# Kernel optimization log

Hardware: AMD Instinct MI355X
Metric: run time of the kernel (lower is better)

## Reference

```python
import jax, jax.numpy as jnp
import numpy as np

B, N, X_DIM, Y_DIM = 256, 128, 8, 8
Z_DIM, R_DIM, HID = 64, 128, 256
STEPS = 50
SIGMA_SQ = 0.5 ** 2
EPSILON = 1.0


def setup_inputs() -> dict:
    key = jax.random.key(0)
    ks = jax.random.split(key, 20)
    s = lambda fan_in: 1.0 / np.sqrt(fan_in)
    inp = {
        'x_ctx': jax.random.normal(ks[0], (B, N, X_DIM), jnp.float32),
        'y_ctx': jax.random.normal(ks[1], (B, N, Y_DIM), jnp.float32),
        'mask': jnp.ones((B, N, 1), jnp.float32),
        'z0': jax.random.normal(ks[2], (B, Z_DIM), jnp.float32),
        'noise': jax.random.normal(ks[3], (STEPS, B, Z_DIM), jnp.float32),
        # encoder: pointwise MLP on [x,y] then masked mean pool, project to r_dim
        'We1': jax.random.normal(ks[4], (X_DIM + Y_DIM, HID), jnp.float32) * s(X_DIM + Y_DIM),
        'be1': jnp.zeros((HID,), jnp.float32),
        'We2': jax.random.normal(ks[5], (HID, R_DIM), jnp.float32) * s(HID),
        'be2': jnp.zeros((R_DIM,), jnp.float32),
        # decoder: MLP([x, z]) -> y per context point
        'Wd1': jax.random.normal(ks[6], (X_DIM + Z_DIM, HID), jnp.float32) * s(X_DIM + Z_DIM),
        'bd1': jnp.zeros((HID,), jnp.float32),
        'Wd2': jax.random.normal(ks[7], (HID, Y_DIM), jnp.float32) * s(HID),
        'bd2': jnp.zeros((Y_DIM,), jnp.float32),
        # drift net: MLP([z, r, t]) -> z_dim
        'Wb1': jax.random.normal(ks[8], (Z_DIM + R_DIM + 1, HID), jnp.float32) * s(Z_DIM + R_DIM + 1),
        'bb1': jnp.zeros((HID,), jnp.float32),
        'Wb2': jax.random.normal(ks[9], (HID, Z_DIM), jnp.float32) * s(HID),
        'bb2': jnp.zeros((Z_DIM,), jnp.float32),
    }
    return inp


def _encode(x, y, mask, We1, be1, We2, be2):
    phi = jax.nn.gelu(jnp.concatenate([x, y], axis=-1) @ We1 + be1)  # [B,N,H]
    pooled = (phi * mask).sum(axis=1) / jnp.maximum(mask.sum(axis=1), 1.0)  # [B,H]
    return pooled @ We2 + be2  # [B,R]


def _decode(z, x, Wd1, bd1, Wd2, bd2):
    zb = jnp.broadcast_to(z[:, None, :], (z.shape[0], x.shape[1], z.shape[1]))
    h = jax.nn.gelu(jnp.concatenate([x, zb], axis=-1) @ Wd1 + bd1)  # [B,N,H]
    return h @ Wd2 + bd2  # [B,N,Y]


def _drift(z, r, t_col, Wb1, bb1, Wb2, bb2):
    h = jax.nn.gelu(jnp.concatenate([z, r, t_col], axis=-1) @ Wb1 + bb1)
    return h @ Wb2 + bb2  # [B,Z]


def reference(x_ctx, y_ctx, mask, z0, noise,
              We1, be1, We2, be2, Wd1, bd1, Wd2, bd2, Wb1, bb1, Wb2, bb2):
    dt = 1.0 / STEPS
    r = _encode(x_ctx, y_ctx, mask, We1, be1, We2, be2)  # [B,R]

    def energy_sum(z, t):
        u0 = 0.5 * jnp.sum(z ** 2, axis=1)  # [B]
        mu_y = _decode(z, x_ctx, Wd1, bd1, Wd2, bd2)
        sse = jnp.sum(((y_ctx - mu_y) ** 2) * mask, axis=(1, 2))  # [B]
        u1 = 0.5 * sse / SIGMA_SQ + u0
        return jnp.sum((1.0 - t) * u0 + t * u1)

    grad_energy = jax.grad(energy_sum, argnums=0)
    t_steps = (jnp.arange(STEPS, dtype=jnp.float32) * dt)
    noise_scale = jnp.sqrt(jnp.float32(2.0 * EPSILON * dt))

    def step(z, xs):
        t_curr, eps_noise = xs
        grad_u = jnp.clip(grad_energy(z, t_curr), -100.0, 100.0)
        t_col = jnp.full((z.shape[0], 1), t_curr, dtype=z.dtype)
        b = _drift(z, r, t_col, Wb1, bb1, Wb2, bb2)
        dz = (-EPSILON * grad_u + b) * dt + noise_scale * eps_noise
        return z + dz, None

    z_final, _ = jax.lax.scan(step, z0, (t_steps, noise))
    return z_final
```

## Files before the change

kernel.cpp:

```cpp
#include <hip/hip_runtime.h>
#include <math.h>

#define BB    256
#define NN_   128
#define ZD    64
#define RD    128
#define HID   256
#define NSTEPS 50
#define NT    16
#define NTILES 8
#define TPB   512
#define PADD  258

__device__ __forceinline__ double fast_exp_d(double x) {
    const double L2E   = 1.44269504088896340736;
    const double LN2HI = 6.93147180369123816490e-01;
    const double LN2LO = 1.90821492927058770002e-10;
    const double MAGIC = 6755399441055744.0;
    double vn = fma(x, L2E, MAGIC);
    int ni = __double2loint(vn);
    double n = vn - MAGIC;
    double r = fma(n, -LN2HI, x);
    r = fma(n, -LN2LO, r);
    double p = 2.50521083854417187751e-08;
    p = fma(p, r, 2.75573192239858906526e-07);
    p = fma(p, r, 2.75573192239858906526e-06);
    p = fma(p, r, 2.48015873015873015873e-05);
    p = fma(p, r, 1.98412698412698412698e-04);
    p = fma(p, r, 1.38888888888888888889e-03);
    p = fma(p, r, 8.33333333333333333333e-03);
    p = fma(p, r, 4.16666666666666666667e-02);
    p = fma(p, r, 1.66666666666666666667e-01);
    p = fma(p, r, 0.5);
    p = fma(p, r, 1.0);
    p = fma(p, r, 1.0);
    return p * __hiloint2double((1023 + ni) << 20, 0);
}

__device__ __forceinline__ double sigmoid_d(double w) {
    double wc = fmin(fmax(w, -60.0), 60.0);
    double e = fast_exp_d(-wc);
    double d = 1.0 + e;
    float r0 = __builtin_amdgcn_rcpf((float)d);
    double y = (double)r0;
    y = fma(y, fma(-d, y, 1.0), y);
    y = fma(y, fma(-d, y, 1.0), y);
    return y;
}

__device__ __forceinline__ double gelu_d(double x) {
    const double c2 = 1.59576912160573071176;
    double w = c2 * x * fma(0.044715, x * x, 1.0);
    return x * sigmoid_d(w);
}

__device__ __forceinline__ void gelu_both_d(double x, double& h, double& gp) {
    const double c  = 0.79788456080286535588;
    const double a  = 0.044715;
    double x2 = x * x;
    double w  = (2.0 * c) * x * fma(a, x2, 1.0);
    double hp = sigmoid_d(w);
    h = x * hp;
    double s = hp * (1.0 - hp);
    gp = fma(x * s, (2.0 * c) * fma(3.0 * a, x2, 1.0), hp);
}

struct Smem {
    double h_t[NT][PADD];
    float  wd2t_f[8][PADD];
    double z_ds[ZD];
    double hb_ds[HID];
    double scratch2[2][HID];
    double pmgz[512];
    double res_r[NT][8];
    double bp_d[8][ZD];
    double bd2_d[8];
    double bb2_d[ZD];
    double hbt_s[HID];
    double wbt_s[HID];
    float  bd1_s[HID];
    float  gp_t[NT][HID];
    float  x_s[NN_][8];
    float  y_s[NN_][8];
    float  m_s[NN_];
    __align__(16) float4 wd1z4[HID][16];
};

__global__ void __launch_bounds__(TPB)
nets_sampler_kernel(
    const float* __restrict__ x_ctx, const float* __restrict__ y_ctx,
    const float* __restrict__ mask,  const float* __restrict__ z0,
    const float* __restrict__ noise,
    const float* __restrict__ We1, const float* __restrict__ be1,
    const float* __restrict__ We2, const float* __restrict__ be2,
    const float* __restrict__ Wd1, const float* __restrict__ bd1,
    const float* __restrict__ Wd2, const float* __restrict__ bd2,
    const float* __restrict__ Wb1, const float* __restrict__ bb1,
    const float* __restrict__ Wb2, const float* __restrict__ bb2,
    float* __restrict__ out)
{
    extern __shared__ char smem_raw[];
    Smem& sm = *reinterpret_cast<Smem*>(smem_raw);

    const int b   = blockIdx.x;
    const int tid = threadIdx.x;
    const int j   = tid & 255;
    const int g   = tid >> 8;
    double* r_d = &sm.res_r[0][0];

    if (tid < 256) {
        reinterpret_cast<float4*>(&sm.x_s[0][0])[tid] =
            reinterpret_cast<const float4*>(x_ctx + (size_t)b * NN_ * 8)[tid];
        reinterpret_cast<float4*>(&sm.y_s[0][0])[tid] =
            reinterpret_cast<const float4*>(y_ctx + (size_t)b * NN_ * 8)[tid];
        sm.bd1_s[j] = bd1[j];
    }
    if (tid < NN_) sm.m_s[tid] = mask[(size_t)b * NN_ + tid];
    if (tid < ZD) {
        sm.z_ds[tid]  = (double)z0[(size_t)b * ZD + tid];
        sm.bb2_d[tid] = (double)bb2[tid];
    }
    if (tid < 8) sm.bd2_d[tid] = (double)bd2[tid];

#pragma unroll
    for (int kk = 0; kk < 32; kk++) {
        const int k = g * 32 + kk;
        const float v = Wd1[(8 + k) * HID + j];
        reinterpret_cast<float*>(&sm.wd1z4[j][0])[4 * ((k >> 2) ^ (j & 15)) + (k & 3)] = v;
    }

    float wd1x[8];
#pragma unroll
    for (int k = 0; k < 8; k++) wd1x[k] = Wd1[k * HID + j];

    const int du_k = tid & 63, du_c = tid >> 6;

    if (g == 0) {
        float4 a0 = reinterpret_cast<const float4*>(Wd2 + (size_t)j * 8)[0];
        float4 a1 = reinterpret_cast<const float4*>(Wd2 + (size_t)j * 8)[1];
        sm.wd2t_f[0][j] = a0.x; sm.wd2t_f[1][j] = a0.y;
        sm.wd2t_f[2][j] = a0.z; sm.wd2t_f[3][j] = a0.w;
        sm.wd2t_f[4][j] = a1.x; sm.wd2t_f[5][j] = a1.y;
        sm.wd2t_f[6][j] = a1.z; sm.wd2t_f[7][j] = a1.w;
    }

    __syncthreads();

    if (tid < 256) {
        float we1r[16];
#pragma unroll
        for (int k = 0; k < 16; k++) we1r[k] = We1[k * HID + j];
        double be1_d = (double)be1[j];
        double msum = 0.0;
        for (int n = 0; n < NN_; n++) msum += (double)sm.m_s[n];
        msum = fmax(msum, 1.0);
        double pacc = 0.0;
        for (int n = 0; n < NN_; n++) {
            double pre = be1_d;
#pragma unroll
            for (int k = 0; k < 8; k++) pre = fma((double)sm.x_s[n][k], (double)we1r[k], pre);
#pragma unroll
            for (int k = 0; k < 8; k++) pre = fma((double)sm.y_s[n][k], (double)we1r[8 + k], pre);
            pacc += gelu_d(pre) * (double)sm.m_s[n];
        }
        sm.hb_ds[j] = pacc / msum;
    }
    __syncthreads();
    if (tid < 256) {
        int i = tid & 127, half = tid >> 7;
        double racc = 0.0;
        for (int jj = half * 128; jj < half * 128 + 128; jj++)
            racc = fma(sm.hb_ds[jj], (double)We2[jj * RD + i], racc);
        sm.scratch2[half][i] = racc;
    }
    __syncthreads();
    if (tid < RD) r_d[tid] = sm.scratch2[0][tid] + sm.scratch2[1][tid] + (double)be2[tid];
    __syncthreads();

    if (tid < 256) {
        double hbr = (double)bb1[j];
        for (int k = 0; k < RD; k++)
            hbr = fma(r_d[k], (double)Wb1[(ZD + k) * HID + j], hbr);
        sm.hbt_s[j] = hbr;
        sm.wbt_s[j] = (double)Wb1[(ZD + RD) * HID + j];
    }
    __syncthreads();

    const double dt  = 1.0 / (double)NSTEPS;
    const double nsc = sqrt(2.0 * 1.0 * dt);

    for (int s = 0; s < NSTEPS; s++) {
        const double t = (double)s * dt;

        float nzf = 0.0f;
        if (tid < ZD) nzf = noise[((size_t)s * BB + b) * ZD + tid];

        double zd0 = 0.0, zd1 = 0.0;
#pragma unroll 4
        for (int q = 0; q < 16; q++) {
            float4 wv = sm.wd1z4[j][q ^ (j & 15)];
            const int k = q * 4;
            zd0 = fma(sm.z_ds[k],     (double)wv.x, zd0);
            zd1 = fma(sm.z_ds[k + 1], (double)wv.y, zd1);
            zd0 = fma(sm.z_ds[k + 2], (double)wv.z, zd0);
            zd1 = fma(sm.z_ds[k + 3], (double)wv.w, zd1);
        }
        const double zpre = (double)sm.bd1_s[j] + zd0 + zd1;

        {
            double a0 = 0.0;
            const int kb = g * 32;
            const float* wb1p = Wb1 + kb * HID + j;
#pragma unroll 8
            for (int kk = 0; kk < 32; kk++)
                a0 = fma(sm.z_ds[kb + kk], (double)wb1p[kk * HID], a0);
            sm.scratch2[g][j] = a0;
        }
        __syncthreads();
        if (tid < 256) {
            double hacc = sm.hbt_s[j] + t * sm.wbt_s[j]
                        + sm.scratch2[0][j] + sm.scratch2[1][j];
            sm.hb_ds[j] = gelu_d(hacc);
        }
        __syncthreads();
        {
            double acc = 0.0;
            const float* wb2p = Wb2 + (du_c * 32) * ZD + du_k;
#pragma unroll 8
            for (int i = 0; i < 32; i++)
                acc = fma(sm.hb_ds[du_c * 32 + i], (double)wb2p[i * ZD], acc);
            sm.bp_d[du_c][du_k] = acc;
        }

        double S = 0.0;
        for (int tile = 0; tile < NTILES; tile++) {
            const int base = tile * NT;
            const int rb = g * 8;
#pragma unroll 2
            for (int nn = 0; nn < 8; nn++) {
                const int row = rb + nn;
                const float4 xa = *reinterpret_cast<const float4*>(&sm.x_s[base + row][0]);
                const float4 xb = *reinterpret_cast<const float4*>(&sm.x_s[base + row][4]);
                double pre = zpre;
                pre = fma((double)xa.x, (double)wd1x[0], pre);
                pre = fma((double)xa.y, (double)wd1x[1], pre);
                pre = fma((double)xa.z, (double)wd1x[2], pre);
                pre = fma((double)xa.w, (double)wd1x[3], pre);
                pre = fma((double)xb.x, (double)wd1x[4], pre);
                pre = fma((double)xb.y, (double)wd1x[5], pre);
                pre = fma((double)xb.z, (double)wd1x[6], pre);
                pre = fma((double)xb.w, (double)wd1x[7], pre);
                double h, gp;
                gelu_both_d(pre, h, gp);
                sm.h_t[row][j]  = h;
                sm.gp_t[row][j] = (float)gp;
            }
            __syncthreads();
            {
                const int q = tid >> 7, pair = tid & 127;
                const int nn = pair >> 3, yd = pair & 7;
                const double2* hrow = reinterpret_cast<const double2*>(&sm.h_t[nn][q * 64]);
                const float2*  wrow = reinterpret_cast<const float2*>(&sm.wd2t_f[yd][q * 64]);
                double a0 = 0.0, a1 = 0.0;
#pragma unroll 8
                for (int i = 0; i < 32; i++) {
                    double2 hv = hrow[i];
                    float2  wv = wrow[i];
                    a0 = fma(hv.x, (double)wv.x, a0);
                    a1 = fma(hv.y, (double)wv.y, a1);
                }
                sm.pmgz[q * 128 + pair] = a0 + a1;
            }
            __syncthreads();
            if (tid < 128) {
                const int nn = tid >> 3, yd = tid & 7;
                double mu = sm.pmgz[tid] + sm.pmgz[128 + tid] + sm.pmgz[256 + tid]
                          + sm.pmgz[384 + tid] + sm.bd2_d[yd];
                sm.res_r[nn][yd] = 4.0 * t * (mu - (double)sm.y_s[base + nn][yd])
                                           * (double)sm.m_s[base + nn];
            }
            __syncthreads();
            {
                const float w0 = sm.wd2t_f[0][j], w1 = sm.wd2t_f[1][j];
                const float w2 = sm.wd2t_f[2][j], w3 = sm.wd2t_f[3][j];
                const float w4 = sm.wd2t_f[4][j], w5 = sm.wd2t_f[5][j];
                const float w6 = sm.wd2t_f[6][j], w7 = sm.wd2t_f[7][j];
                const int rb2 = g * 8;
#pragma unroll 2
                for (int nn = 0; nn < 8; nn++) {
                    const int row = rb2 + nn;
                    const double2* rr = reinterpret_cast<const double2*>(&sm.res_r[row][0]);
                    double2 r0 = rr[0], r1 = rr[1], r2 = rr[2], r3 = rr[3];
                    double dh = r0.x * (double)w0 + r0.y * (double)w1
                              + r1.x * (double)w2 + r1.y * (double)w3
                              + r2.x * (double)w4 + r2.y * (double)w5
                              + r3.x * (double)w6 + r3.y * (double)w7;
                    S = fma(dh, (double)sm.gp_t[row][j], S);
                }
            }
            __syncthreads();
        }

        sm.scratch2[g][j] = S;
        __syncthreads();
        {
            const int k = du_k, c = du_c;
            const int qk = k >> 2, ck = k & 3;
            double acc = 0.0;
#pragma unroll 8
            for (int i = 0; i < 32; i++) {
                const int jj = c * 32 + i;
                const float w = reinterpret_cast<const float*>(&sm.wd1z4[jj][0])
                                    [4 * (qk ^ (jj & 15)) + ck];
                const double sv = sm.scratch2[0][jj] + sm.scratch2[1][jj];
                acc = fma(sv, (double)w, acc);
            }
            sm.pmgz[c * 64 + k] = acc;
        }
        __syncthreads();
        if (tid < ZD) {
            double gsum = sm.z_ds[tid];
#pragma unroll
            for (int c = 0; c < 8; c++) gsum += sm.pmgz[c * 64 + tid];
            gsum = fmin(fmax(gsum, -100.0), 100.0);
            double bdr = sm.bb2_d[tid];
#pragma unroll
            for (int c = 0; c < 8; c++) bdr += sm.bp_d[c][tid];
            sm.z_ds[tid] = sm.z_ds[tid] + (bdr - gsum) * dt + nsc * (double)nzf;
        }
        __syncthreads();
    }

    if (tid < ZD) out[(size_t)b * ZD + tid] = (float)sm.z_ds[tid];
}

extern "C" void kernel_launch(void* const* d_in, const int* in_sizes, int n_in,
                              void* d_out, int out_size, void* d_ws, size_t ws_size,
                              hipStream_t stream) {
    const float* x_ctx = (const float*)d_in[0];
    const float* y_ctx = (const float*)d_in[1];
    const float* maskp = (const float*)d_in[2];
    const float* z0    = (const float*)d_in[3];
    const float* noise = (const float*)d_in[4];
    const float* We1   = (const float*)d_in[5];
    const float* be1   = (const float*)d_in[6];
    const float* We2   = (const float*)d_in[7];
    const float* be2   = (const float*)d_in[8];
    const float* Wd1   = (const float*)d_in[9];
    const float* bd1   = (const float*)d_in[10];
    const float* Wd2   = (const float*)d_in[11];
    const float* bd2   = (const float*)d_in[12];
    const float* Wb1   = (const float*)d_in[13];
    const float* bb1   = (const float*)d_in[14];
    const float* Wb2   = (const float*)d_in[15];
    const float* bb2   = (const float*)d_in[16];
    float* out = (float*)d_out;

    (void)hipFuncSetAttribute((const void*)nets_sampler_kernel,
                              hipFuncAttributeMaxDynamicSharedMemorySize,
                              (int)sizeof(Smem));

    nets_sampler_kernel<<<BB, TPB, sizeof(Smem), stream>>>(
        x_ctx, y_ctx, maskp, z0, noise,
        We1, be1, We2, be2, Wd1, bd1, Wd2, bd2, Wb1, bb1, Wb2, bb2, out);
}
```

Baseline: 1.859 ms.

## Double block size to 1024 threads and repartition per-step work

```diff
diff --git a/kernel.cpp b/kernel.cpp
--- a/kernel.cpp
+++ b/kernel.cpp
@@ -9,7 +9,7 @@
 #define NSTEPS 50
 #define NT    16
 #define NTILES 8
-#define TPB   512
+#define TPB   1024
 #define PADD  258
 
 __device__ __forceinline__ double fast_exp_d(double x) {
@@ -70,16 +70,15 @@
     float  wd2t_f[8][PADD];
     double z_ds[ZD];
     double hb_ds[HID];
-    double scratch2[2][HID];
-    double pmgz[512];
+    double scratch4[4][HID];
+    double pmgz[1024];
     double res_r[NT][8];
-    double bp_d[8][ZD];
+    double bp_d[16][ZD];
     double bd2_d[8];
     double bb2_d[ZD];
     double hbt_s[HID];
     double wbt_s[HID];
     float  bd1_s[HID];
-    float  gp_t[NT][HID];
     float  x_s[NN_][8];
     float  y_s[NN_][8];
     float  m_s[NN_];
@@ -105,7 +104,8 @@
     const int b   = blockIdx.x;
     const int tid = threadIdx.x;
     const int j   = tid & 255;
-    const int g   = tid >> 8;
+    const int q2  = tid >> 8;
+    const int du_k = tid & 63, du_c = tid >> 6;
     double* r_d = &sm.res_r[0][0];
 
     if (tid < 256) {
@@ -114,28 +114,6 @@
         reinterpret_cast<float4*>(&sm.y_s[0][0])[tid] =
             reinterpret_cast<const float4*>(y_ctx + (size_t)b * NN_ * 8)[tid];
         sm.bd1_s[j] = bd1[j];
-    }
-    if (tid < NN_) sm.m_s[tid] = mask[(size_t)b * NN_ + tid];
-    if (tid < ZD) {
-        sm.z_ds[tid]  = (double)z0[(size_t)b * ZD + tid];
-        sm.bb2_d[tid] = (double)bb2[tid];
-    }
-    if (tid < 8) sm.bd2_d[tid] = (double)bd2[tid];
-
-#pragma unroll
-    for (int kk = 0; kk < 32; kk++) {
-        const int k = g * 32 + kk;
-        const float v = Wd1[(8 + k) * HID + j];
-        reinterpret_cast<float*>(&sm.wd1z4[j][0])[4 * ((k >> 2) ^ (j & 15)) + (k & 3)] = v;
-    }
-
-    float wd1x[8];
-#pragma unroll
-    for (int k = 0; k < 8; k++) wd1x[k] = Wd1[k * HID + j];
-
-    const int du_k = tid & 63, du_c = tid >> 6;
-
-    if (g == 0) {
         float4 a0 = reinterpret_cast<const float4*>(Wd2 + (size_t)j * 8)[0];
         float4 a1 = reinterpret_cast<const float4*>(Wd2 + (size_t)j * 8)[1];
         sm.wd2t_f[0][j] = a0.x; sm.wd2t_f[1][j] = a0.y;
@@ -143,6 +121,23 @@
         sm.wd2t_f[4][j] = a1.x; sm.wd2t_f[5][j] = a1.y;
         sm.wd2t_f[6][j] = a1.z; sm.wd2t_f[7][j] = a1.w;
     }
+    if (tid < NN_) sm.m_s[tid] = mask[(size_t)b * NN_ + tid];
+    if (tid < ZD) {
+        sm.z_ds[tid]  = (double)z0[(size_t)b * ZD + tid];
+        sm.bb2_d[tid] = (double)bb2[tid];
+    }
+    if (tid < 8) sm.bd2_d[tid] = (double)bd2[tid];
+
+#pragma unroll
+    for (int kk = 0; kk < 16; kk++) {
+        const int k = q2 * 16 + kk;
+        const float v = Wd1[(8 + k) * HID + j];
+        reinterpret_cast<float*>(&sm.wd1z4[j][0])[4 * ((k >> 2) ^ (j & 15)) + (k & 3)] = v;
+    }
+
+    float wd1x[8];
+#pragma unroll
+    for (int k = 0; k < 8; k++) wd1x[k] = Wd1[k * HID + j];
 
     __syncthreads();
 
@@ -171,10 +166,10 @@
         double racc = 0.0;
         for (int jj = half * 128; jj < half * 128 + 128; jj++)
             racc = fma(sm.hb_ds[jj], (double)We2[jj * RD + i], racc);
-        sm.scratch2[half][i] = racc;
+        sm.scratch4[half][i] = racc;
     }
     __syncthreads();
-    if (tid < RD) r_d[tid] = sm.scratch2[0][tid] + sm.scratch2[1][tid] + (double)be2[tid];
+    if (tid < RD) r_d[tid] = sm.scratch4[0][tid] + sm.scratch4[1][tid] + (double)be2[tid];
     __syncthreads();
 
     if (tid < 256) {
@@ -209,61 +204,101 @@
 
         {
             double a0 = 0.0;
-            const int kb = g * 32;
+            const int kb = q2 * 16;
             const float* wb1p = Wb1 + kb * HID + j;
 #pragma unroll 8
-            for (int kk = 0; kk < 32; kk++)
+            for (int kk = 0; kk < 16; kk++)
                 a0 = fma(sm.z_ds[kb + kk], (double)wb1p[kk * HID], a0);
-            sm.scratch2[g][j] = a0;
+            sm.scratch4[q2][j] = a0;
         }
         __syncthreads();
         if (tid < 256) {
             double hacc = sm.hbt_s[j] + t * sm.wbt_s[j]
-                        + sm.scratch2[0][j] + sm.scratch2[1][j];
+                        + sm.scratch4[0][j] + sm.scratch4[1][j]
+                        + sm.scratch4[2][j] + sm.scratch4[3][j];
             sm.hb_ds[j] = gelu_d(hacc);
         }
         __syncthreads();
         {
             double acc = 0.0;
-            const float* wb2p = Wb2 + (du_c * 32) * ZD + du_k;
+            const float* wb2p = Wb2 + (du_c * 16) * ZD + du_k;
 #pragma unroll 8
-            for (int i = 0; i < 32; i++)
-                acc = fma(sm.hb_ds[du_c * 32 + i], (double)wb2p[i * ZD], acc);
+            for (int i = 0; i < 16; i++)
+                acc = fma(sm.hb_ds[du_c * 16 + i], (double)wb2p[i * ZD], acc);
             sm.bp_d[du_c][du_k] = acc;
         }
 
         double S = 0.0;
+        const int rb = q2 * 4;
+        float gp_r0, gp_r1, gp_r2, gp_r3;
+
         for (int tile = 0; tile < NTILES; tile++) {
-            const int base = tile * NT;
-            const int rb = g * 8;
-#pragma unroll 2
-            for (int nn = 0; nn < 8; nn++) {
-                const int row = rb + nn;
-                const float4 xa = *reinterpret_cast<const float4*>(&sm.x_s[base + row][0]);
-                const float4 xb = *reinterpret_cast<const float4*>(&sm.x_s[base + row][4]);
-                double pre = zpre;
-                pre = fma((double)xa.x, (double)wd1x[0], pre);
-                pre = fma((double)xa.y, (double)wd1x[1], pre);
-                pre = fma((double)xa.z, (double)wd1x[2], pre);
-                pre = fma((double)xa.w, (double)wd1x[3], pre);
-                pre = fma((double)xb.x, (double)wd1x[4], pre);
-                pre = fma((double)xb.y, (double)wd1x[5], pre);
-                pre = fma((double)xb.z, (double)wd1x[6], pre);
-                pre = fma((double)xb.w, (double)wd1x[7], pre);
-                double h, gp;
-                gelu_both_d(pre, h, gp);
-                sm.h_t[row][j]  = h;
-                sm.gp_t[row][j] = (float)gp;
+            const int xb = tile * NT + rb;
+            {
+                const float4 xa = *reinterpret_cast<const float4*>(&sm.x_s[xb + 0][0]);
+                const float4 xxb = *reinterpret_cast<const float4*>(&sm.x_s[xb + 0][4]);
+                const float4 xc = *reinterpret_cast<const float4*>(&sm.x_s[xb + 1][0]);
+                const float4 xd = *reinterpret_cast<const float4*>(&sm.x_s[xb + 1][4]);
+                double p0 = zpre, p1 = zpre;
+                p0 = fma((double)xa.x, (double)wd1x[0], p0);
+                p0 = fma((double)xa.y, (double)wd1x[1], p0);
+                p0 = fma((double)xa.z, (double)wd1x[2], p0);
+                p0 = fma((double)xa.w, (double)wd1x[3], p0);
+                p0 = fma((double)xxb.x, (double)wd1x[4], p0);
+                p0 = fma((double)xxb.y, (double)wd1x[5], p0);
+                p0 = fma((double)xxb.z, (double)wd1x[6], p0);
+                p0 = fma((double)xxb.w, (double)wd1x[7], p0);
+                p1 = fma((double)xc.x, (double)wd1x[0], p1);
+                p1 = fma((double)xc.y, (double)wd1x[1], p1);
+                p1 = fma((double)xc.z, (double)wd1x[2], p1);
+                p1 = fma((double)xc.w, (double)wd1x[3], p1);
+                p1 = fma((double)xd.x, (double)wd1x[4], p1);
+                p1 = fma((double)xd.y, (double)wd1x[5], p1);
+                p1 = fma((double)xd.z, (double)wd1x[6], p1);
+                p1 = fma((double)xd.w, (double)wd1x[7], p1);
+                double h0, g0, h1, g1;
+                gelu_both_d(p0, h0, g0);
+                gelu_both_d(p1, h1, g1);
+                sm.h_t[rb + 0][j] = h0; gp_r0 = (float)g0;
+                sm.h_t[rb + 1][j] = h1; gp_r1 = (float)g1;
+            }
+            {
+                const float4 xa = *reinterpret_cast<const float4*>(&sm.x_s[xb + 2][0]);
+                const float4 xxb = *reinterpret_cast<const float4*>(&sm.x_s[xb + 2][4]);
+                const float4 xc = *reinterpret_cast<const float4*>(&sm.x_s[xb + 3][0]);
+                const float4 xd = *reinterpret_cast<const float4*>(&sm.x_s[xb + 3][4]);
+                double p0 = zpre, p1 = zpre;
+                p0 = fma((double)xa.x, (double)wd1x[0], p0);
+                p0 = fma((double)xa.y, (double)wd1x[1], p0);
+                p0 = fma((double)xa.z, (double)wd1x[2], p0);
+                p0 = fma((double)xa.w, (double)wd1x[3], p0);
+                p0 = fma((double)xxb.x, (double)wd1x[4], p0);
+                p0 = fma((double)xxb.y, (double)wd1x[5], p0);
+                p0 = fma((double)xxb.z, (double)wd1x[6], p0);
+                p0 = fma((double)xxb.w, (double)wd1x[7], p0);
+                p1 = fma((double)xc.x, (double)wd1x[0], p1);
+                p1 = fma((double)xc.y, (double)wd1x[1], p1);
+                p1 = fma((double)xc.z, (double)wd1x[2], p1);
+                p1 = fma((double)xc.w, (double)wd1x[3], p1);
+                p1 = fma((double)xd.x, (double)wd1x[4], p1);
+                p1 = fma((double)xd.y, (double)wd1x[5], p1);
+                p1 = fma((double)xd.z, (double)wd1x[6], p1);
+                p1 = fma((double)xd.w, (double)wd1x[7], p1);
+                double h0, g0, h1, g1;
+                gelu_both_d(p0, h0, g0);
+                gelu_both_d(p1, h1, g1);
+                sm.h_t[rb + 2][j] = h0; gp_r2 = (float)g0;
+                sm.h_t[rb + 3][j] = h1; gp_r3 = (float)g1;
             }
             __syncthreads();
             {
                 const int q = tid >> 7, pair = tid & 127;
                 const int nn = pair >> 3, yd = pair & 7;
-                const double2* hrow = reinterpret_cast<const double2*>(&sm.h_t[nn][q * 64]);
-                const float2*  wrow = reinterpret_cast<const float2*>(&sm.wd2t_f[yd][q * 64]);
+                const double2* hrow = reinterpret_cast<const double2*>(&sm.h_t[nn][q * 32]);
+                const float2*  wrow = reinterpret_cast<const float2*>(&sm.wd2t_f[yd][q * 32]);
                 double a0 = 0.0, a1 = 0.0;
 #pragma unroll 8
-                for (int i = 0; i < 32; i++) {
+                for (int i = 0; i < 16; i++) {
                     double2 hv = hrow[i];
                     float2  wv = wrow[i];
                     a0 = fma(hv.x, (double)wv.x, a0);
@@ -274,10 +309,11 @@
             __syncthreads();
             if (tid < 128) {
                 const int nn = tid >> 3, yd = tid & 7;
-                double mu = sm.pmgz[tid] + sm.pmgz[128 + tid] + sm.pmgz[256 + tid]
-                          + sm.pmgz[384 + tid] + sm.bd2_d[yd];
-                sm.res_r[nn][yd] = 4.0 * t * (mu - (double)sm.y_s[base + nn][yd])
-                                           * (double)sm.m_s[base + nn];
+                double mu = sm.bd2_d[yd];
+#pragma unroll
+                for (int q = 0; q < 8; q++) mu += sm.pmgz[q * 128 + tid];
+                sm.res_r[nn][yd] = 4.0 * t * (mu - (double)sm.y_s[tile * NT + nn][yd])
+                                           * (double)sm.m_s[tile * NT + nn];
             }
             __syncthreads();
             {
@@ -285,34 +321,51 @@
                 const float w2 = sm.wd2t_f[2][j], w3 = sm.wd2t_f[3][j];
                 const float w4 = sm.wd2t_f[4][j], w5 = sm.wd2t_f[5][j];
                 const float w6 = sm.wd2t_f[6][j], w7 = sm.wd2t_f[7][j];
-                const int rb2 = g * 8;
-#pragma unroll 2
-                for (int nn = 0; nn < 8; nn++) {
-                    const int row = rb2 + nn;
-                    const double2* rr = reinterpret_cast<const double2*>(&sm.res_r[row][0]);
-                    double2 r0 = rr[0], r1 = rr[1], r2 = rr[2], r3 = rr[3];
-                    double dh = r0.x * (double)w0 + r0.y * (double)w1
-                              + r1.x * (double)w2 + r1.y * (double)w3
-                              + r2.x * (double)w4 + r2.y * (double)w5
-                              + r3.x * (double)w6 + r3.y * (double)w7;
-                    S = fma(dh, (double)sm.gp_t[row][j], S);
-                }
-            }
-            __syncthreads();
-        }
-
-        sm.scratch2[g][j] = S;
+                const double2* rr0 = reinterpret_cast<const double2*>(&sm.res_r[rb + 0][0]);
+                const double2* rr1 = reinterpret_cast<const double2*>(&sm.res_r[rb + 1][0]);
+                const double2* rr2 = reinterpret_cast<const double2*>(&sm.res_r[rb + 2][0]);
+                const double2* rr3 = reinterpret_cast<const double2*>(&sm.res_r[rb + 3][0]);
+                double2 a0, a1, a2, a3;
+                a0 = rr0[0]; a1 = rr0[1]; a2 = rr0[2]; a3 = rr0[3];
+                double dh0 = a0.x * (double)w0 + a0.y * (double)w1
+                           + a1.x * (double)w2 + a1.y * (double)w3
+                           + a2.x * (double)w4 + a2.y * (double)w5
+                           + a3.x * (double)w6 + a3.y * (double)w7;
+                S = fma(dh0, (double)gp_r0, S);
+                a0 = rr1[0]; a1 = rr1[1]; a2 = rr1[2]; a3 = rr1[3];
+                double dh1 = a0.x * (double)w0 + a0.y * (double)w1
+                           + a1.x * (double)w2 + a1.y * (double)w3
+                           + a2.x * (double)w4 + a2.y * (double)w5
+                           + a3.x * (double)w6 + a3.y * (double)w7;
+                S = fma(dh1, (double)gp_r1, S);
+                a0 = rr2[0]; a1 = rr2[1]; a2 = rr2[2]; a3 = rr2[3];
+                double dh2 = a0.x * (double)w0 + a0.y * (double)w1
+                           + a1.x * (double)w2 + a1.y * (double)w3
+                           + a2.x * (double)w4 + a2.y * (double)w5
+                           + a3.x * (double)w6 + a3.y * (double)w7;
+                S = fma(dh2, (double)gp_r2, S);
+                a0 = rr3[0]; a1 = rr3[1]; a2 = rr3[2]; a3 = rr3[3];
+                double dh3 = a0.x * (double)w0 + a0.y * (double)w1
+                           + a1.x * (double)w2 + a1.y * (double)w3
+                           + a2.x * (double)w4 + a2.y * (double)w5
+                           + a3.x * (double)w6 + a3.y * (double)w7;
+                S = fma(dh3, (double)gp_r3, S);
+            }
+        }
+
+        sm.scratch4[q2][j] = S;
         __syncthreads();
         {
             const int k = du_k, c = du_c;
             const int qk = k >> 2, ck = k & 3;
             double acc = 0.0;
 #pragma unroll 8
-            for (int i = 0; i < 32; i++) {
-                const int jj = c * 32 + i;
+            for (int i = 0; i < 16; i++) {
+                const int jj = c * 16 + i;
                 const float w = reinterpret_cast<const float*>(&sm.wd1z4[jj][0])
                                     [4 * (qk ^ (jj & 15)) + ck];
-                const double sv = sm.scratch2[0][jj] + sm.scratch2[1][jj];
+                const double sv = sm.scratch4[0][jj] + sm.scratch4[1][jj]
+                                + sm.scratch4[2][jj] + sm.scratch4[3][jj];
                 acc = fma(sv, (double)w, acc);
             }
             sm.pmgz[c * 64 + k] = acc;
@@ -321,11 +374,11 @@
         if (tid < ZD) {
             double gsum = sm.z_ds[tid];
 #pragma unroll
-            for (int c = 0; c < 8; c++) gsum += sm.pmgz[c * 64 + tid];
+            for (int c = 0; c < 16; c++) gsum += sm.pmgz[c * 64 + tid];
             gsum = fmin(fmax(gsum, -100.0), 100.0);
             double bdr = sm.bb2_d[tid];
 #pragma unroll
-            for (int c = 0; c < 8; c++) bdr += sm.bp_d[c][tid];
+            for (int c = 0; c < 16; c++) bdr += sm.bp_d[c][tid];
             sm.z_ds[tid] = sm.z_ds[tid] + (bdr - gsum) * dt + nsc * (double)nzf;
         }
         __syncthreads();
```

After: 1.782 ms. 1.04x faster.
